# Performance work log

Hardware: AMD Instinct MI355X
Metric: run time of the kernel (lower is better)

Reference implementation:

```python
import jax, jax.numpy as jnp
import numpy as np

D_K = 16

def setup_inputs() -> dict:
    key = jax.random.key(0)
    kq, kk, kv, km, kb = jax.random.split(key, 5)
    B, H, S, d = 8, 16, 1024, D_K
    Q = jax.random.normal(kq, (B, H, S, d), dtype=jnp.float32)
    K = jax.random.normal(kk, (B, H, S, d), dtype=jnp.float32)
    V = jax.random.normal(kv, (B, H, S, d), dtype=jnp.float32)
    attn_mask = jax.random.randint(km, (B, 1, S, S), 0, 2).astype(jnp.bool_)
    MD_bias = jax.random.normal(kb, (B, 1, S, S), dtype=jnp.float32)
    return {"Q": Q, "K": K, "V": V, "attn_mask": attn_mask, "MD_bias": MD_bias}

def reference(Q, K, V, attn_mask, MD_bias):
    # scores: [B,H,S,S] = Q K^T / sqrt(d_k) + MD_bias, masked to -1e9
    scale = 1.0 / np.sqrt(D_K).astype(np.float32)
    scores = jnp.einsum('bhqd,bhkd->bhqk', Q, K) * scale + MD_bias
    scores = jnp.where(attn_mask, jnp.float32(-1e9), scores)
    attn = jax.nn.softmax(scores, axis=-1)
    context = jnp.einsum('bhqk,bhkd->bhqd', attn, V)
    return context
```

## Files before the change

### kernel.cpp

```cpp
#include <hip/hip_runtime.h>
#include <hip/hip_fp16.h>
#include <math.h>

#define SEQ    1024
#define DK     16
#define NHEAD  16
#define NBATCH 8
#define LOG2E  1.4426950408889634f

#define CH     128
#define NCH    (SEQ / CH)
#define KHL_STRIDE 72
#define VT_STRIDE  272
#define KHL_CH (CH * KHL_STRIDE)
#define VT_CH  (DK * VT_STRIDE)
#define BUF_SZ (KHL_CH + VT_CH)

typedef __attribute__((ext_vector_type(4))) short  short4v;
typedef __attribute__((ext_vector_type(4))) float  float4v;
typedef __attribute__((ext_vector_type(2))) unsigned int uint2v;

static __device__ __forceinline__ float fast_exp2(float x) {
#if __has_builtin(__builtin_amdgcn_exp2f)
    return __builtin_amdgcn_exp2f(x);
#else
    return exp2f(x);
#endif
}

static __device__ __forceinline__ float4v mfma16(short4v a, short4v b, float4v c) {
#if __has_builtin(__builtin_amdgcn_mfma_f32_16x16x16bf16_1k)
    return __builtin_amdgcn_mfma_f32_16x16x16bf16_1k(a, b, c, 0, 0, 0);
#else
    float4v d = c;
    asm volatile("v_mfma_f32_16x16x16_bf16 %0, %1, %2, %0" : "+v"(d) : "v"(a), "v"(b));
    return d;
#endif
}

static __device__ __forceinline__ unsigned bf16_rne(float x) {
    unsigned u = __float_as_uint(x);
    return (u + 0x7FFFu + ((u >> 16) & 1u)) >> 16;
}
static __device__ __forceinline__ float bf16_to_f(unsigned b) {
    return __uint_as_float(b << 16);
}
static __device__ __forceinline__ short4v bc_s4(unsigned lo, unsigned hi) {
    uint2v u; u.x = lo; u.y = hi;
    return __builtin_bit_cast(short4v, u);
}
static __device__ __forceinline__ unsigned h2pack(int m0, float b0, int m1, float b1) {
    const __half2 a = __floats2half2_rn(m0 ? -60000.f : b0 * LOG2E,
                                        m1 ? -60000.f : b1 * LOG2E);
    return __builtin_bit_cast(unsigned, a);
}

__global__ __launch_bounds__(256)
void prep_all(const float* __restrict__ K, const float* __restrict__ V,
              const int* __restrict__ mask, const float* __restrict__ bias,
              uint4* __restrict__ KHL, short* __restrict__ Vt,
              uint4* __restrict__ biasp) {
    const int blk = blockIdx.x;
    if (blk < 2048) {
        const int i4 = blk * 256 + threadIdx.x;
        const float4 k = ((const float4*)K)[i4];
        const float w[4] = {k.x, k.y, k.z, k.w};
        unsigned hh[4], ll[4];
        #pragma unroll
        for (int e = 0; e < 4; ++e) {
            hh[e] = bf16_rne(w[e]);
            ll[e] = bf16_rne(w[e] - bf16_to_f(hh[e]));
        }
        uint4 o;
        o.x = hh[0] | (hh[1] << 16);
        o.y = hh[2] | (hh[3] << 16);
        o.z = ll[0] | (ll[1] << 16);
        o.w = ll[2] | (ll[3] << 16);
        KHL[i4] = o;
    } else if (blk < 4096) {
        __shared__ float Vs[64][17];
        const int t  = threadIdx.x;
        const int bb = blk - 2048;
        const int bh = bb >> 4;
        const int s0 = (bb & 15) * 64;
        {
            const int row = t >> 2, c4 = t & 3;
            const float4 v = ((const float4*)V)[((size_t)bh * SEQ + s0 + row) * 4 + c4];
            Vs[row][c4 * 4 + 0] = v.x; Vs[row][c4 * 4 + 1] = v.y;
            Vs[row][c4 * 4 + 2] = v.z; Vs[row][c4 * 4 + 3] = v.w;
        }
        __syncthreads();
        const int d = t >> 4, sg = t & 15;
        short4v o;
        #pragma unroll
        for (int i = 0; i < 4; ++i) o[i] = (short)bf16_rne(Vs[sg * 4 + i][d]);
        ((short4v*)Vt)[(((size_t)bh * DK + d) * SEQ + s0) / 4 + sg] = o;
    } else {
        __shared__ uint4 BsT[64][16];
        const int t    = threadIdx.x;
        const int blk2 = blk - 4096;
        const int b    = blk2 >> 7;
        const int qt64 = (blk2 >> 3) & 15;
        const int c    = blk2 & 7;
        #pragma unroll
        for (int i = 0; i < 8; ++i) {
            const int idx = t + i * 256;
            const int row = idx >> 5;
            const int c4  = idx & 31;
            const size_t ga = ((size_t)b * SEQ + qt64 * 64 + row) * SEQ + c * 128 + c4 * 4;
            const float4 bv = *(const float4*)(bias + ga);
            const int4   mv = *(const int4*)(mask + ga);
            uint2 u;
            u.x = h2pack(mv.x, bv.x, mv.y, bv.y);
            u.y = h2pack(mv.z, bv.z, mv.w, bv.w);
            const int j = c4 >> 1;
            ((uint2*)&BsT[row][j ^ (row & 15)])[c4 & 1] = u;
        }
        __syncthreads();
        const int w = t >> 6, lane = t & 63, n = lane & 15, g = lane >> 4;
        #pragma unroll
        for (int tp = 0; tp < 4; ++tp) {
            const int j = tp * 4 + g;
            const uint4 v = BsT[w * 16 + n][j ^ n];
            const size_t ob = ((((size_t)(b * 16 + qt64) * 4 + w) * 8 + c) * 4 + tp) * 64 + lane;
            biasp[ob] = v;
        }
    }
}

__global__ __launch_bounds__(256, 4)
void sdpa_flash(const float* __restrict__ Q, const uint4* __restrict__ KHL,
                const short* __restrict__ Vt, const uint4* __restrict__ biasp,
                float* __restrict__ out) {
    __shared__ __align__(16) char smem[2][BUF_SZ];

    const int tid  = threadIdx.x;
    const int wave = tid >> 6;
    const int lane = tid & 63;
    const int n    = lane & 15;
    const int g    = lane >> 4;
    const int permn = ((n >> 2) << 3) | (n & 3);

    const int b  = blockIdx.x & 7;
    const int j  = blockIdx.x >> 3;
    const int qt = j & 7;
    const int h  = j >> 3;
    const int q0 = qt * 128;

    const size_t bh = (size_t)b * NHEAD + h;

    short4v qh[2], ql[2];
    size_t  bfbase[2];
    #pragma unroll
    for (int f = 0; f < 2; ++f) {
        const int qrow = q0 + f * 64 + wave * 16 + n;
        const float4 qv = *(const float4*)(Q + (bh * SEQ + qrow) * DK + g * 4);
        const float qsc = 0.25f * LOG2E;
        const float v[4] = {qv.x * qsc, qv.y * qsc, qv.z * qsc, qv.w * qsc};
        #pragma unroll
        for (int e = 0; e < 4; ++e) {
            const unsigned hu = bf16_rne(v[e]);
            qh[f][e] = (short)hu;
            ql[f][e] = (short)bf16_rne(v[e] - bf16_to_f(hu));
        }
        bfbase[f] = (((size_t)(b * 16 + qt * 2 + f) * 4 + wave) * 32) * 64 + lane;
    }

    const uint4* KHLh = KHL + bh * SEQ * 4;
    const uint4* VtH  = (const uint4*)(Vt + bh * DK * SEQ);

    float4v acc[2];
    float   lsum[2] = {0.f, 0.f};
    acc[0] = (float4v){0.f, 0.f, 0.f, 0.f};
    acc[1] = (float4v){0.f, 0.f, 0.f, 0.f};

    uint4 st0, st1, st2;
    {
        st0 = KHLh[tid];
        st1 = KHLh[256 + tid];
        st2 = VtH[(tid >> 4) * 128 + (tid & 15)];
        char* s = smem[0];
        *(uint4*)(s + (tid >> 2) * KHL_STRIDE + (tid & 3) * 16) = st0;
        const int e = tid + 256;
        *(uint4*)(s + (e >> 2) * KHL_STRIDE + (e & 3) * 16) = st1;
        *(uint4*)(s + KHL_CH + (tid >> 4) * VT_STRIDE + (tid & 15) * 16) = st2;
    }
    __syncthreads();

    for (int c = 0; c < NCH; ++c) {
        const int cur = c & 1;
        if (c < NCH - 1) {
            const uint4* kg = KHLh + (c + 1) * 512;
            st0 = kg[tid];
            st1 = kg[256 + tid];
            st2 = VtH[(tid >> 4) * 128 + (c + 1) * 16 + (tid & 15)];
        }
        uint4 bb[2][4];
        #pragma unroll
        for (int f = 0; f < 2; ++f)
            #pragma unroll
            for (int tp = 0; tp < 4; ++tp)
                bb[f][tp] = biasp[bfbase[f] + (size_t)(c * 4 + tp) * 64];

        const char* khl = smem[cur];
        const char* vtl = smem[cur] + KHL_CH;

        #pragma unroll
        for (int tp = 0; tp < 4; ++tp) {
            const int rowA = tp * 32 + permn;
            const uint4 kA = *(const uint4*)(khl + rowA * KHL_STRIDE + g * 16);
            const uint4 kB = *(const uint4*)(khl + (rowA + 4) * KHL_STRIDE + g * 16);
            const uint4 vv = *(const uint4*)(vtl + n * VT_STRIDE + tp * 64 + g * 16);
            const short4v khiA = bc_s4(kA.x, kA.y), kloA = bc_s4(kA.z, kA.w);
            const short4v khiB = bc_s4(kB.x, kB.y), kloB = bc_s4(kB.z, kB.w);
            const short4v vtA  = bc_s4(vv.x, vv.y), vtB  = bc_s4(vv.z, vv.w);

            #pragma unroll
            for (int f = 0; f < 2; ++f) {
                {
                    const float2 f01 = __half22float2(__builtin_bit_cast(__half2, bb[f][tp].x));
                    const float2 f23 = __half22float2(__builtin_bit_cast(__half2, bb[f][tp].y));
                    float4v s; s[0] = f01.x; s[1] = f01.y; s[2] = f23.x; s[3] = f23.y;
                    s = mfma16(khiA, qh[f], s);
                    s = mfma16(kloA, qh[f], s);
                    s = mfma16(khiA, ql[f], s);
                    const float p0 = fast_exp2(s[0]), p1 = fast_exp2(s[1]);
                    const float p2 = fast_exp2(s[2]), p3 = fast_exp2(s[3]);
                    lsum[f] += (p0 + p1) + (p2 + p3);
                    const unsigned u0 = __float_as_uint(p0) + 0x8000u;
                    const unsigned u1 = __float_as_uint(p1) + 0x8000u;
                    const unsigned u2 = __float_as_uint(p2) + 0x8000u;
                    const unsigned u3 = __float_as_uint(p3) + 0x8000u;
                    const short4v pf = bc_s4((u1 & 0xFFFF0000u) | (u0 >> 16),
                                             (u3 & 0xFFFF0000u) | (u2 >> 16));
                    acc[f] = mfma16(pf, vtA, acc[f]);
                }
                {
                    const float2 f01 = __half22float2(__builtin_bit_cast(__half2, bb[f][tp].z));
                    const float2 f23 = __half22float2(__builtin_bit_cast(__half2, bb[f][tp].w));
                    float4v s; s[0] = f01.x; s[1] = f01.y; s[2] = f23.x; s[3] = f23.y;
                    s = mfma16(khiB, qh[f], s);
                    s = mfma16(kloB, qh[f], s);
                    s = mfma16(khiB, ql[f], s);
                    const float p0 = fast_exp2(s[0]), p1 = fast_exp2(s[1]);
                    const float p2 = fast_exp2(s[2]), p3 = fast_exp2(s[3]);
                    lsum[f] += (p0 + p1) + (p2 + p3);
                    const unsigned u0 = __float_as_uint(p0) + 0x8000u;
                    const unsigned u1 = __float_as_uint(p1) + 0x8000u;
                    const unsigned u2 = __float_as_uint(p2) + 0x8000u;
                    const unsigned u3 = __float_as_uint(p3) + 0x8000u;
                    const short4v pf = bc_s4((u1 & 0xFFFF0000u) | (u0 >> 16),
                                             (u3 & 0xFFFF0000u) | (u2 >> 16));
                    acc[f] = mfma16(pf, vtB, acc[f]);
                }
            }
        }

        if (c < NCH - 1) {
            char* s = smem[cur ^ 1];
            *(uint4*)(s + (tid >> 2) * KHL_STRIDE + (tid & 3) * 16) = st0;
            const int e = tid + 256;
            *(uint4*)(s + (e >> 2) * KHL_STRIDE + (e & 3) * 16) = st1;
            *(uint4*)(s + KHL_CH + (tid >> 4) * VT_STRIDE + (tid & 15) * 16) = st2;
        }
        __syncthreads();
    }

    #pragma unroll
    for (int f = 0; f < 2; ++f) {
        float l = lsum[f];
        l += __shfl_xor(l, 16, 64);
        l += __shfl_xor(l, 32, 64);
        const float inv = 1.0f / l;
        const size_t obase = bh * SEQ + q0 + f * 64 + wave * 16;
        #pragma unroll
        for (int r = 0; r < 4; ++r) {
            const float invr = __shfl(inv, 4 * g + r, 64);
            out[(obase + 4 * g + r) * DK + n] = acc[f][r] * invr;
        }
    }
}

#define FTQ 256
#define FTK 32
__global__ __launch_bounds__(256, 2)
void sdpa_fallback(const float* __restrict__ Q, const float* __restrict__ K,
                   const float* __restrict__ V, const int* __restrict__ mask,
                   const float* __restrict__ bias, float* __restrict__ out) {
    __shared__ float Ks[FTK][DK];
    __shared__ float Vs[FTK][DK];
    __shared__ float Bsf[FTQ][FTK + 1];

    const int tid = threadIdx.x;
    const int blk = blockIdx.x;
    const int h   = blk & (NHEAD - 1);
    const int qt  = (blk >> 4) & 3;
    const int b   = blk >> 6;
    const int q0  = qt * FTQ;
    const float qscale = 0.25f * LOG2E;
    const size_t bh = (size_t)b * NHEAD + h;

    float Qr[DK];
    {
        const float4* q4 = (const float4*)(Q + (bh * SEQ + q0 + tid) * DK);
        #pragma unroll
        for (int i = 0; i < 4; ++i) {
            float4 v = q4[i];
            Qr[4*i+0] = v.x * qscale; Qr[4*i+1] = v.y * qscale;
            Qr[4*i+2] = v.z * qscale; Qr[4*i+3] = v.w * qscale;
        }
    }
    float acc[DK];
    #pragma unroll
    for (int d = 0; d < DK; ++d) acc[d] = 0.0f;
    float l = 0.0f;

    const float* Kbase = K + bh * SEQ * DK;
    const float* Vbase = V + bh * SEQ * DK;
    const float* Bbase = bias + ((size_t)b * SEQ + q0) * SEQ;
    const int*   Mbase = mask + ((size_t)b * SEQ + q0) * SEQ;

    for (int t = 0; t < SEQ / FTK; ++t) {
        const int k0 = t * FTK;
        if (tid < 128) {
            float4 kv = ((const float4*)(Kbase + (size_t)k0 * DK))[tid];
            float4 vv = ((const float4*)(Vbase + (size_t)k0 * DK))[tid];
            ((float4*)&Ks[0][0])[tid] = kv;
            ((float4*)&Vs[0][0])[tid] = vv;
        }
        #pragma unroll
        for (int i = 0; i < 8; ++i) {
            int e4 = tid + i * 256, row = e4 >> 3, c4 = e4 & 7;
            const float4 bv = *(const float4*)(Bbase + (size_t)row * SEQ + k0 + c4 * 4);
            const int4   mv = *(const int4*)  (Mbase + (size_t)row * SEQ + k0 + c4 * 4);
            float* dst = &Bsf[row][c4 * 4];
            dst[0] = mv.x ? -1e9f : bv.x * LOG2E;
            dst[1] = mv.y ? -1e9f : bv.y * LOG2E;
            dst[2] = mv.z ? -1e9f : bv.z * LOG2E;
            dst[3] = mv.w ? -1e9f : bv.w * LOG2E;
        }
        __syncthreads();
        #pragma unroll 4
        for (int kk = 0; kk < FTK; ++kk) {
            float s = Bsf[tid][kk];
            const float4 k0v = *(const float4*)&Ks[kk][0];
            const float4 k1v = *(const float4*)&Ks[kk][4];
            const float4 k2v = *(const float4*)&Ks[kk][8];
            const float4 k3v = *(const float4*)&Ks[kk][12];
            s = fmaf(Qr[0],  k0v.x, s); s = fmaf(Qr[1],  k0v.y, s);
            s = fmaf(Qr[2],  k0v.z, s); s = fmaf(Qr[3],  k0v.w, s);
            s = fmaf(Qr[4],  k1v.x, s); s = fmaf(Qr[5],  k1v.y, s);
            s = fmaf(Qr[6],  k1v.z, s); s = fmaf(Qr[7],  k1v.w, s);
            s = fmaf(Qr[8],  k2v.x, s); s = fmaf(Qr[9],  k2v.y, s);
            s = fmaf(Qr[10], k2v.z, s); s = fmaf(Qr[11], k2v.w, s);
            s = fmaf(Qr[12], k3v.x, s); s = fmaf(Qr[13], k3v.y, s);
            s = fmaf(Qr[14], k3v.z, s); s = fmaf(Qr[15], k3v.w, s);
            float p = fast_exp2(s);
            l += p;
            const float4 v0 = *(const float4*)&Vs[kk][0];
            const float4 v1 = *(const float4*)&Vs[kk][4];
            const float4 v2 = *(const float4*)&Vs[kk][8];
            const float4 v3 = *(const float4*)&Vs[kk][12];
            acc[0]  = fmaf(p, v0.x, acc[0]);  acc[1]  = fmaf(p, v0.y, acc[1]);
            acc[2]  = fmaf(p, v0.z, acc[2]);  acc[3]  = fmaf(p, v0.w, acc[3]);
            acc[4]  = fmaf(p, v1.x, acc[4]);  acc[5]  = fmaf(p, v1.y, acc[5]);
            acc[6]  = fmaf(p, v1.z, acc[6]);  acc[7]  = fmaf(p, v1.w, acc[7]);
            acc[8]  = fmaf(p, v2.x, acc[8]);  acc[9]  = fmaf(p, v2.y, acc[9]);
            acc[10] = fmaf(p, v2.z, acc[10]); acc[11] = fmaf(p, v2.w, acc[11]);
            acc[12] = fmaf(p, v3.x, acc[12]); acc[13] = fmaf(p, v3.y, acc[13]);
            acc[14] = fmaf(p, v3.z, acc[14]); acc[15] = fmaf(p, v3.w, acc[15]);
        }
        __syncthreads();
    }
    const float inv = 1.0f / l;
    float4* o4 = (float4*)(out + (bh * SEQ + q0 + tid) * DK);
    #pragma unroll
    for (int i = 0; i < 4; ++i) {
        float4 v;
        v.x = acc[4*i+0] * inv; v.y = acc[4*i+1] * inv;
        v.z = acc[4*i+2] * inv; v.w = acc[4*i+3] * inv;
        o4[i] = v;
    }
}

extern "C" void kernel_launch(void* const* d_in, const int* in_sizes, int n_in,
                              void* d_out, int out_size, void* d_ws, size_t ws_size,
                              hipStream_t stream) {
    const float* Q    = (const float*)d_in[0];
    const float* K    = (const float*)d_in[1];
    const float* V    = (const float*)d_in[2];
    const int*   mask = (const int*)  d_in[3];
    const float* bias = (const float*)d_in[4];
    float* out = (float*)d_out;

    const size_t nKeys    = (size_t)NBATCH * NHEAD * SEQ;
    const size_t khlBytes = nKeys * 64;
    const size_t vtBytes  = nKeys * DK * sizeof(short);
    const size_t bpBytes  = (size_t)NBATCH * SEQ * SEQ * 2;
    const size_t need     = khlBytes + vtBytes + bpBytes;

    if (ws_size >= need) {
        char* w = (char*)d_ws;
        uint4* KHL   = (uint4*)(w);
        short* Vt    = (short*)(w + khlBytes);
        uint4* biasp = (uint4*)(w + khlBytes + vtBytes);

        prep_all<<<5120, 256, 0, stream>>>(K, V, mask, bias, KHL, Vt, biasp);
        sdpa_flash<<<1024, 256, 0, stream>>>(Q, KHL, Vt, biasp, out);
    } else {
        sdpa_fallback<<<NBATCH * NHEAD * (SEQ / FTQ), FTQ, 0, stream>>>(Q, K, V, mask, bias, out);
    }
}
```

Measured before the change: 169.1 us.

## Fuse K/V bf16 conversion into flash kernel staging; shrink bias prep kernel

Removes the K hi/lo split and V transpose passes from the prep kernel. The flash kernel now loads fp32 K and V directly, converts them to bf16 (hi/lo for K, transposed for V) while staging each chunk into LDS, and no longer round-trips through workspace. The prep kernel now only packs mask and bias, with 2048 smaller blocks and a narrower swizzled LDS tile. The softmax probabilities now use the packed bf16 convert instruction where available. The cost is extra conversion ALU work inside the main loop, plus double the fp32 K/V global reads in the flash kernel, since each head's K/V is reloaded by 8 query-tile blocks.

Measured after the change: 164.3 us. 2.8% less time.

```diff
diff --git a/kernel.cpp b/kernel.cpp
--- a/kernel.cpp
+++ b/kernel.cpp
@@ -17,6 +17,7 @@
 #define BUF_SZ (KHL_CH + VT_CH)
 
 typedef __attribute__((ext_vector_type(4))) short  short4v;
+typedef __attribute__((ext_vector_type(2))) short  short2v;
 typedef __attribute__((ext_vector_type(4))) float  float4v;
 typedef __attribute__((ext_vector_type(2))) unsigned int uint2v;
 
@@ -45,6 +46,14 @@
 static __device__ __forceinline__ float bf16_to_f(unsigned b) {
     return __uint_as_float(b << 16);
 }
+static __device__ __forceinline__ unsigned pk_bf16(float a, float b) {
+#if __has_builtin(__builtin_amdgcn_cvt_pk_bf16_f32)
+    short2v r = __builtin_amdgcn_cvt_pk_bf16_f32(a, b);
+    return __builtin_bit_cast(unsigned, r);
+#else
+    return bf16_rne(a) | (bf16_rne(b) << 16);
+#endif
+}
 static __device__ __forceinline__ short4v bc_s4(unsigned lo, unsigned hi) {
     uint2v u; u.x = lo; u.y = hi;
     return __builtin_bit_cast(short4v, u);
@@ -56,81 +65,47 @@
 }
 
 __global__ __launch_bounds__(256)
-void prep_all(const float* __restrict__ K, const float* __restrict__ V,
-              const int* __restrict__ mask, const float* __restrict__ bias,
-              uint4* __restrict__ KHL, short* __restrict__ Vt,
-              uint4* __restrict__ biasp) {
-    const int blk = blockIdx.x;
-    if (blk < 2048) {
-        const int i4 = blk * 256 + threadIdx.x;
-        const float4 k = ((const float4*)K)[i4];
-        const float w[4] = {k.x, k.y, k.z, k.w};
-        unsigned hh[4], ll[4];
-        #pragma unroll
-        for (int e = 0; e < 4; ++e) {
-            hh[e] = bf16_rne(w[e]);
-            ll[e] = bf16_rne(w[e] - bf16_to_f(hh[e]));
-        }
-        uint4 o;
-        o.x = hh[0] | (hh[1] << 16);
-        o.y = hh[2] | (hh[3] << 16);
-        o.z = ll[0] | (ll[1] << 16);
-        o.w = ll[2] | (ll[3] << 16);
-        KHL[i4] = o;
-    } else if (blk < 4096) {
-        __shared__ float Vs[64][17];
-        const int t  = threadIdx.x;
-        const int bb = blk - 2048;
-        const int bh = bb >> 4;
-        const int s0 = (bb & 15) * 64;
-        {
-            const int row = t >> 2, c4 = t & 3;
-            const float4 v = ((const float4*)V)[((size_t)bh * SEQ + s0 + row) * 4 + c4];
-            Vs[row][c4 * 4 + 0] = v.x; Vs[row][c4 * 4 + 1] = v.y;
-            Vs[row][c4 * 4 + 2] = v.z; Vs[row][c4 * 4 + 3] = v.w;
-        }
-        __syncthreads();
-        const int d = t >> 4, sg = t & 15;
-        short4v o;
-        #pragma unroll
-        for (int i = 0; i < 4; ++i) o[i] = (short)bf16_rne(Vs[sg * 4 + i][d]);
-        ((short4v*)Vt)[(((size_t)bh * DK + d) * SEQ + s0) / 4 + sg] = o;
-    } else {
-        __shared__ uint4 BsT[64][16];
-        const int t    = threadIdx.x;
-        const int blk2 = blk - 4096;
-        const int b    = blk2 >> 7;
-        const int qt64 = (blk2 >> 3) & 15;
-        const int c    = blk2 & 7;
-        #pragma unroll
-        for (int i = 0; i < 8; ++i) {
-            const int idx = t + i * 256;
-            const int row = idx >> 5;
-            const int c4  = idx & 31;
-            const size_t ga = ((size_t)b * SEQ + qt64 * 64 + row) * SEQ + c * 128 + c4 * 4;
-            const float4 bv = *(const float4*)(bias + ga);
-            const int4   mv = *(const int4*)(mask + ga);
-            uint2 u;
-            u.x = h2pack(mv.x, bv.x, mv.y, bv.y);
-            u.y = h2pack(mv.z, bv.z, mv.w, bv.w);
-            const int j = c4 >> 1;
-            ((uint2*)&BsT[row][j ^ (row & 15)])[c4 & 1] = u;
-        }
-        __syncthreads();
-        const int w = t >> 6, lane = t & 63, n = lane & 15, g = lane >> 4;
-        #pragma unroll
-        for (int tp = 0; tp < 4; ++tp) {
-            const int j = tp * 4 + g;
-            const uint4 v = BsT[w * 16 + n][j ^ n];
-            const size_t ob = ((((size_t)(b * 16 + qt64) * 4 + w) * 8 + c) * 4 + tp) * 64 + lane;
-            biasp[ob] = v;
-        }
+void prep_bias(const int* __restrict__ mask, const float* __restrict__ bias,
+               uint4* __restrict__ biasp) {
+    __shared__ uint4 BsT[64][9];
+    const int t    = threadIdx.x;
+    const int blk  = blockIdx.x;
+    const int b    = blk >> 8;
+    const int qt64 = (blk >> 4) & 15;
+    const int c    = (blk >> 1) & 7;
+    const int half = blk & 1;
+    const int kb   = c * 128 + half * 64;
+
+    #pragma unroll
+    for (int i = 0; i < 4; ++i) {
+        const int idx = t + i * 256;
+        const int row = idx >> 4;
+        const int c4  = idx & 15;
+        const size_t ga = ((size_t)b * SEQ + qt64 * 64 + row) * SEQ + kb + c4 * 4;
+        const float4 bv = *(const float4*)(bias + ga);
+        const int4   mv = *(const int4*)(mask + ga);
+        uint2 u;
+        u.x = h2pack(mv.x, bv.x, mv.y, bv.y);
+        u.y = h2pack(mv.z, bv.z, mv.w, bv.w);
+        const int j = c4 >> 1;
+        ((uint2*)&BsT[row][j ^ (row & 7)])[c4 & 1] = u;
+    }
+    __syncthreads();
+    const int w = t >> 6, lane = t & 63, n = lane & 15, g = lane >> 4;
+    const int row = w * 16 + n;
+    #pragma unroll
+    for (int tpl = 0; tpl < 2; ++tpl) {
+        const int tp = half * 2 + tpl;
+        const int jj = tpl * 4 + g;
+        const uint4 v = BsT[row][jj ^ (row & 7)];
+        const size_t ob = ((((size_t)(b * 16 + qt64) * 4 + w) * 8 + c) * 4 + tp) * 64 + lane;
+        biasp[ob] = v;
     }
 }
 
 __global__ __launch_bounds__(256, 4)
-void sdpa_flash(const float* __restrict__ Q, const uint4* __restrict__ KHL,
-                const short* __restrict__ Vt, const uint4* __restrict__ biasp,
+void sdpa_flash(const float* __restrict__ Q, const float* __restrict__ K,
+                const float* __restrict__ V, const uint4* __restrict__ biasp,
                 float* __restrict__ out) {
     __shared__ __align__(16) char smem[2][BUF_SZ];
 
@@ -166,34 +141,67 @@
         bfbase[f] = (((size_t)(b * 16 + qt * 2 + f) * 4 + wave) * 32) * 64 + lane;
     }
 
-    const uint4* KHLh = KHL + bh * SEQ * 4;
-    const uint4* VtH  = (const uint4*)(Vt + bh * DK * SEQ);
+    const float4* Kf4 = (const float4*)(K + bh * SEQ * DK);
+    const float4* Vf4 = (const float4*)(V + bh * SEQ * DK);
+
+    const int sp = tid >> 2;
+    const int cc = tid & 3;
 
     float4v acc[2];
     float   lsum[2] = {0.f, 0.f};
     acc[0] = (float4v){0.f, 0.f, 0.f, 0.f};
     acc[1] = (float4v){0.f, 0.f, 0.f, 0.f};
 
-    uint4 st0, st1, st2;
-    {
-        st0 = KHLh[tid];
-        st1 = KHLh[256 + tid];
-        st2 = VtH[(tid >> 4) * 128 + (tid & 15)];
-        char* s = smem[0];
-        *(uint4*)(s + (tid >> 2) * KHL_STRIDE + (tid & 3) * 16) = st0;
-        const int e = tid + 256;
-        *(uint4*)(s + (e >> 2) * KHL_STRIDE + (e & 3) * 16) = st1;
-        *(uint4*)(s + KHL_CH + (tid >> 4) * VT_STRIDE + (tid & 15) * 16) = st2;
-    }
+    float4 kst0, kst1, vst0, vst1;
+    kst0 = Kf4[tid];
+    kst1 = Kf4[256 + tid];
+    vst0 = Vf4[(2 * sp) * 4 + cc];
+    vst1 = Vf4[(2 * sp + 1) * 4 + cc];
+
+    auto stage = [&](char* s) {
+        {
+            const float w0[4] = {kst0.x, kst0.y, kst0.z, kst0.w};
+            uint4 o;
+            o.x = pk_bf16(w0[0], w0[1]);
+            o.y = pk_bf16(w0[2], w0[3]);
+            o.z = pk_bf16(w0[0] - bf16_to_f(o.x & 0xFFFFu),
+                          w0[1] - bf16_to_f(o.x >> 16));
+            o.w = pk_bf16(w0[2] - bf16_to_f(o.y & 0xFFFFu),
+                          w0[3] - bf16_to_f(o.y >> 16));
+            *(uint4*)(s + (tid >> 2) * KHL_STRIDE + (tid & 3) * 16) = o;
+            const float w1[4] = {kst1.x, kst1.y, kst1.z, kst1.w};
+            uint4 p;
+            p.x = pk_bf16(w1[0], w1[1]);
+            p.y = pk_bf16(w1[2], w1[3]);
+            p.z = pk_bf16(w1[0] - bf16_to_f(p.x & 0xFFFFu),
+                          w1[1] - bf16_to_f(p.x >> 16));
+            p.w = pk_bf16(w1[2] - bf16_to_f(p.y & 0xFFFFu),
+                          w1[3] - bf16_to_f(p.y >> 16));
+            const int e = tid + 256;
+            *(uint4*)(s + (e >> 2) * KHL_STRIDE + (e & 3) * 16) = p;
+        }
+        {
+            const float a0[4] = {vst0.x, vst0.y, vst0.z, vst0.w};
+            const float a1[4] = {vst1.x, vst1.y, vst1.z, vst1.w};
+            #pragma unroll
+            for (int dp = 0; dp < 4; ++dp) {
+                const unsigned pr = pk_bf16(a0[dp], a1[dp]);
+                *(unsigned*)(s + KHL_CH + (cc * 4 + dp) * VT_STRIDE + sp * 4) = pr;
+            }
+        }
+    };
+
+    stage(smem[0]);
     __syncthreads();
 
     for (int c = 0; c < NCH; ++c) {
         const int cur = c & 1;
         if (c < NCH - 1) {
-            const uint4* kg = KHLh + (c + 1) * 512;
-            st0 = kg[tid];
-            st1 = kg[256 + tid];
-            st2 = VtH[(tid >> 4) * 128 + (c + 1) * 16 + (tid & 15)];
+            const int o4 = (c + 1) * 512;
+            kst0 = Kf4[o4 + tid];
+            kst1 = Kf4[o4 + 256 + tid];
+            vst0 = Vf4[o4 + (2 * sp) * 4 + cc];
+            vst1 = Vf4[o4 + (2 * sp + 1) * 4 + cc];
         }
         uint4 bb[2][4];
         #pragma unroll
@@ -227,12 +235,7 @@
                     const float p0 = fast_exp2(s[0]), p1 = fast_exp2(s[1]);
                     const float p2 = fast_exp2(s[2]), p3 = fast_exp2(s[3]);
                     lsum[f] += (p0 + p1) + (p2 + p3);
-                    const unsigned u0 = __float_as_uint(p0) + 0x8000u;
-                    const unsigned u1 = __float_as_uint(p1) + 0x8000u;
-                    const unsigned u2 = __float_as_uint(p2) + 0x8000u;
-                    const unsigned u3 = __float_as_uint(p3) + 0x8000u;
-                    const short4v pf = bc_s4((u1 & 0xFFFF0000u) | (u0 >> 16),
-                                             (u3 & 0xFFFF0000u) | (u2 >> 16));
+                    const short4v pf = bc_s4(pk_bf16(p0, p1), pk_bf16(p2, p3));
                     acc[f] = mfma16(pf, vtA, acc[f]);
                 }
                 {
@@ -245,24 +248,13 @@
                     const float p0 = fast_exp2(s[0]), p1 = fast_exp2(s[1]);
                     const float p2 = fast_exp2(s[2]), p3 = fast_exp2(s[3]);
                     lsum[f] += (p0 + p1) + (p2 + p3);
-                    const unsigned u0 = __float_as_uint(p0) + 0x8000u;
-                    const unsigned u1 = __float_as_uint(p1) + 0x8000u;
-                    const unsigned u2 = __float_as_uint(p2) + 0x8000u;
-                    const unsigned u3 = __float_as_uint(p3) + 0x8000u;
-                    const short4v pf = bc_s4((u1 & 0xFFFF0000u) | (u0 >> 16),
-                                             (u3 & 0xFFFF0000u) | (u2 >> 16));
+                    const short4v pf = bc_s4(pk_bf16(p0, p1), pk_bf16(p2, p3));
                     acc[f] = mfma16(pf, vtB, acc[f]);
                 }
             }
         }
 
-        if (c < NCH - 1) {
-            char* s = smem[cur ^ 1];
-            *(uint4*)(s + (tid >> 2) * KHL_STRIDE + (tid & 3) * 16) = st0;
-            const int e = tid + 256;
-            *(uint4*)(s + (e >> 2) * KHL_STRIDE + (e & 3) * 16) = st1;
-            *(uint4*)(s + KHL_CH + (tid >> 4) * VT_STRIDE + (tid & 15) * 16) = st2;
-        }
+        if (c < NCH - 1) stage(smem[cur ^ 1]);
         __syncthreads();
     }
 
@@ -393,20 +385,12 @@
     const float* bias = (const float*)d_in[4];
     float* out = (float*)d_out;
 
-    const size_t nKeys    = (size_t)NBATCH * NHEAD * SEQ;
-    const size_t khlBytes = nKeys * 64;
-    const size_t vtBytes  = nKeys * DK * sizeof(short);
-    const size_t bpBytes  = (size_t)NBATCH * SEQ * SEQ * 2;
-    const size_t need     = khlBytes + vtBytes + bpBytes;
-
-    if (ws_size >= need) {
-        char* w = (char*)d_ws;
-        uint4* KHL   = (uint4*)(w);
-        short* Vt    = (short*)(w + khlBytes);
-        uint4* biasp = (uint4*)(w + khlBytes + vtBytes);
-
-        prep_all<<<5120, 256, 0, stream>>>(K, V, mask, bias, KHL, Vt, biasp);
-        sdpa_flash<<<1024, 256, 0, stream>>>(Q, KHL, Vt, biasp, out);
+    const size_t bpBytes = (size_t)NBATCH * SEQ * SEQ * 2;
+
+    if (ws_size >= bpBytes) {
+        uint4* biasp = (uint4*)d_ws;
+        prep_bias<<<2048, 256, 0, stream>>>(mask, bias, biasp);
+        sdpa_flash<<<1024, 256, 0, stream>>>(Q, K, V, biasp, out);
     } else {
         sdpa_fallback<<<NBATCH * NHEAD * (SEQ / FTQ), FTQ, 0, stream>>>(Q, K, V, mask, bias, out);
     }
```

## Halve flash tile sizes, compute row sums via MFMA, use packed bf16 convert

Applied to the files above, without the earlier changes.

The flash kernel now handles 64 query rows per block instead of 128 and streams 64-key chunks instead of 128. This doubles the grid and raises the occupancy target to 8 blocks per CU, while reducing registers and shared memory per block. The softmax denominator is now accumulated by an extra MFMA against a ones vector rather than by VALU adds plus cross-lane shuffles. Probabilities are packed with a hardware cvt_pk_bf16 instruction where available. The bias-prep blocks are split in half to match the new layout, which adds more prep blocks and more per-chunk barriers.

After: 200.3 us. 1.18x slower.

```diff
diff --git a/kernel.cpp b/kernel.cpp
--- a/kernel.cpp
+++ b/kernel.cpp
@@ -8,15 +8,16 @@
 #define NBATCH 8
 #define LOG2E  1.4426950408889634f
 
-#define CH     128
+#define CH     64
 #define NCH    (SEQ / CH)
 #define KHL_STRIDE 72
-#define VT_STRIDE  272
+#define VT_STRIDE  144
 #define KHL_CH (CH * KHL_STRIDE)
 #define VT_CH  (DK * VT_STRIDE)
 #define BUF_SZ (KHL_CH + VT_CH)
 
 typedef __attribute__((ext_vector_type(4))) short  short4v;
+typedef __attribute__((ext_vector_type(2))) short  short2v;
 typedef __attribute__((ext_vector_type(4))) float  float4v;
 typedef __attribute__((ext_vector_type(2))) unsigned int uint2v;
 
@@ -44,6 +45,14 @@
 }
 static __device__ __forceinline__ float bf16_to_f(unsigned b) {
     return __uint_as_float(b << 16);
+}
+static __device__ __forceinline__ unsigned pk_bf16(float a, float b) {
+#if __has_builtin(__builtin_amdgcn_cvt_pk_bf16_f32)
+    short2v r = __builtin_amdgcn_cvt_pk_bf16_f32(a, b);
+    return __builtin_bit_cast(unsigned, r);
+#else
+    return bf16_rne(a) | (bf16_rne(b) << 16);
+#endif
 }
 static __device__ __forceinline__ short4v bc_s4(unsigned lo, unsigned hi) {
     uint2v u; u.x = lo; u.y = hi;
@@ -65,17 +74,11 @@
         const int i4 = blk * 256 + threadIdx.x;
         const float4 k = ((const float4*)K)[i4];
         const float w[4] = {k.x, k.y, k.z, k.w};
-        unsigned hh[4], ll[4];
-        #pragma unroll
-        for (int e = 0; e < 4; ++e) {
-            hh[e] = bf16_rne(w[e]);
-            ll[e] = bf16_rne(w[e] - bf16_to_f(hh[e]));
-        }
         uint4 o;
-        o.x = hh[0] | (hh[1] << 16);
-        o.y = hh[2] | (hh[3] << 16);
-        o.z = ll[0] | (ll[1] << 16);
-        o.w = ll[2] | (ll[3] << 16);
+        o.x = pk_bf16(w[0], w[1]);
+        o.y = pk_bf16(w[2], w[3]);
+        o.z = pk_bf16(w[0] - bf16_to_f(o.x & 0xFFFFu), w[1] - bf16_to_f(o.x >> 16));
+        o.w = pk_bf16(w[2] - bf16_to_f(o.y & 0xFFFFu), w[3] - bf16_to_f(o.y >> 16));
         KHL[i4] = o;
     } else if (blk < 4096) {
         __shared__ float Vs[64][17];
@@ -96,39 +99,44 @@
         for (int i = 0; i < 4; ++i) o[i] = (short)bf16_rne(Vs[sg * 4 + i][d]);
         ((short4v*)Vt)[(((size_t)bh * DK + d) * SEQ + s0) / 4 + sg] = o;
     } else {
-        __shared__ uint4 BsT[64][16];
+        __shared__ uint4 BsT[64][9];
         const int t    = threadIdx.x;
         const int blk2 = blk - 4096;
-        const int b    = blk2 >> 7;
-        const int qt64 = (blk2 >> 3) & 15;
-        const int c    = blk2 & 7;
-        #pragma unroll
-        for (int i = 0; i < 8; ++i) {
+        const int b    = blk2 >> 8;
+        const int qt64 = (blk2 >> 4) & 15;
+        const int c    = (blk2 >> 1) & 7;
+        const int half = blk2 & 1;
+        const int kb   = c * 128 + half * 64;
+
+        #pragma unroll
+        for (int i = 0; i < 4; ++i) {
             const int idx = t + i * 256;
-            const int row = idx >> 5;
-            const int c4  = idx & 31;
-            const size_t ga = ((size_t)b * SEQ + qt64 * 64 + row) * SEQ + c * 128 + c4 * 4;
+            const int row = idx >> 4;
+            const int c4  = idx & 15;
+            const size_t ga = ((size_t)b * SEQ + qt64 * 64 + row) * SEQ + kb + c4 * 4;
             const float4 bv = *(const float4*)(bias + ga);
             const int4   mv = *(const int4*)(mask + ga);
             uint2 u;
             u.x = h2pack(mv.x, bv.x, mv.y, bv.y);
             u.y = h2pack(mv.z, bv.z, mv.w, bv.w);
             const int j = c4 >> 1;
-            ((uint2*)&BsT[row][j ^ (row & 15)])[c4 & 1] = u;
+            ((uint2*)&BsT[row][j ^ (row & 7)])[c4 & 1] = u;
         }
         __syncthreads();
         const int w = t >> 6, lane = t & 63, n = lane & 15, g = lane >> 4;
-        #pragma unroll
-        for (int tp = 0; tp < 4; ++tp) {
-            const int j = tp * 4 + g;
-            const uint4 v = BsT[w * 16 + n][j ^ n];
+        const int row = w * 16 + n;
+        #pragma unroll
+        for (int tpl = 0; tpl < 2; ++tpl) {
+            const int tp = half * 2 + tpl;
+            const int jj = tpl * 4 + g;
+            const uint4 v = BsT[row][jj ^ (row & 7)];
             const size_t ob = ((((size_t)(b * 16 + qt64) * 4 + w) * 8 + c) * 4 + tp) * 64 + lane;
             biasp[ob] = v;
         }
     }
 }
 
-__global__ __launch_bounds__(256, 4)
+__global__ __launch_bounds__(256, 8)
 void sdpa_flash(const float* __restrict__ Q, const uint4* __restrict__ KHL,
                 const short* __restrict__ Vt, const uint4* __restrict__ biasp,
                 float* __restrict__ out) {
@@ -143,70 +151,64 @@
 
     const int b  = blockIdx.x & 7;
     const int j  = blockIdx.x >> 3;
-    const int qt = j & 7;
-    const int h  = j >> 3;
-    const int q0 = qt * 128;
-
-    const size_t bh = (size_t)b * NHEAD + h;
-
-    short4v qh[2], ql[2];
-    size_t  bfbase[2];
-    #pragma unroll
-    for (int f = 0; f < 2; ++f) {
-        const int qrow = q0 + f * 64 + wave * 16 + n;
+    const int qt = j & 15;
+    const int h  = j >> 4;
+    const int q0 = qt * 64;
+
+    const size_t bh   = (size_t)b * NHEAD + h;
+    const int    qrow = q0 + wave * 16 + n;
+
+    short4v qh, ql;
+    {
         const float4 qv = *(const float4*)(Q + (bh * SEQ + qrow) * DK + g * 4);
         const float qsc = 0.25f * LOG2E;
         const float v[4] = {qv.x * qsc, qv.y * qsc, qv.z * qsc, qv.w * qsc};
         #pragma unroll
         for (int e = 0; e < 4; ++e) {
             const unsigned hu = bf16_rne(v[e]);
-            qh[f][e] = (short)hu;
-            ql[f][e] = (short)bf16_rne(v[e] - bf16_to_f(hu));
-        }
-        bfbase[f] = (((size_t)(b * 16 + qt * 2 + f) * 4 + wave) * 32) * 64 + lane;
-    }
+            qh[e] = (short)hu;
+            ql[e] = (short)bf16_rne(v[e] - bf16_to_f(hu));
+        }
+    }
+    const size_t bfbase = (((size_t)(b * 16 + qt) * 4 + wave) * 32) * 64 + lane;
 
     const uint4* KHLh = KHL + bh * SEQ * 4;
     const uint4* VtH  = (const uint4*)(Vt + bh * DK * SEQ);
 
-    float4v acc[2];
-    float   lsum[2] = {0.f, 0.f};
-    acc[0] = (float4v){0.f, 0.f, 0.f, 0.f};
-    acc[1] = (float4v){0.f, 0.f, 0.f, 0.f};
-
-    uint4 st0, st1, st2;
-    {
-        st0 = KHLh[tid];
-        st1 = KHLh[256 + tid];
-        st2 = VtH[(tid >> 4) * 128 + (tid & 15)];
-        char* s = smem[0];
-        *(uint4*)(s + (tid >> 2) * KHL_STRIDE + (tid & 3) * 16) = st0;
-        const int e = tid + 256;
-        *(uint4*)(s + (e >> 2) * KHL_STRIDE + (e & 3) * 16) = st1;
-        *(uint4*)(s + KHL_CH + (tid >> 4) * VT_STRIDE + (tid & 15) * 16) = st2;
-    }
+    const int vd = tid >> 3, vc = tid & 7;
+
+    float4v acc   = (float4v){0.f, 0.f, 0.f, 0.f};
+    float4v acc_l = (float4v){0.f, 0.f, 0.f, 0.f};
+    const short4v kOnes = {(short)0x3F80, (short)0x3F80, (short)0x3F80, (short)0x3F80};
+
+    uint4 kst, vst;
+    kst = KHLh[tid];
+    if (tid < 128) vst = VtH[vd * 128 + vc];
+
+    auto stage = [&](char* s) {
+        *(uint4*)(s + (tid >> 2) * KHL_STRIDE + (tid & 3) * 16) = kst;
+        if (tid < 128)
+            *(uint4*)(s + KHL_CH + vd * VT_STRIDE + vc * 16) = vst;
+    };
+
+    stage(smem[0]);
     __syncthreads();
 
     for (int c = 0; c < NCH; ++c) {
         const int cur = c & 1;
         if (c < NCH - 1) {
-            const uint4* kg = KHLh + (c + 1) * 512;
-            st0 = kg[tid];
-            st1 = kg[256 + tid];
-            st2 = VtH[(tid >> 4) * 128 + (c + 1) * 16 + (tid & 15)];
-        }
-        uint4 bb[2][4];
-        #pragma unroll
-        for (int f = 0; f < 2; ++f)
-            #pragma unroll
-            for (int tp = 0; tp < 4; ++tp)
-                bb[f][tp] = biasp[bfbase[f] + (size_t)(c * 4 + tp) * 64];
+            kst = KHLh[(c + 1) * 256 + tid];
+            if (tid < 128) vst = VtH[vd * 128 + (c + 1) * 8 + vc];
+        }
+        uint4 bb[2];
+        bb[0] = biasp[bfbase + (size_t)(c * 2 + 0) * 64];
+        bb[1] = biasp[bfbase + (size_t)(c * 2 + 1) * 64];
 
         const char* khl = smem[cur];
         const char* vtl = smem[cur] + KHL_CH;
 
         #pragma unroll
-        for (int tp = 0; tp < 4; ++tp) {
+        for (int tp = 0; tp < 2; ++tp) {
             const int rowA = tp * 32 + permn;
             const uint4 kA = *(const uint4*)(khl + rowA * KHL_STRIDE + g * 16);
             const uint4 kB = *(const uint4*)(khl + (rowA + 4) * KHL_STRIDE + g * 16);
@@ -215,69 +217,43 @@
             const short4v khiB = bc_s4(kB.x, kB.y), kloB = bc_s4(kB.z, kB.w);
             const short4v vtA  = bc_s4(vv.x, vv.y), vtB  = bc_s4(vv.z, vv.w);
 
-            #pragma unroll
-            for (int f = 0; f < 2; ++f) {
-                {
-                    const float2 f01 = __half22float2(__builtin_bit_cast(__half2, bb[f][tp].x));
-                    const float2 f23 = __half22float2(__builtin_bit_cast(__half2, bb[f][tp].y));
-                    float4v s; s[0] = f01.x; s[1] = f01.y; s[2] = f23.x; s[3] = f23.y;
-                    s = mfma16(khiA, qh[f], s);
-                    s = mfma16(kloA, qh[f], s);
-                    s = mfma16(khiA, ql[f], s);
-                    const float p0 = fast_exp2(s[0]), p1 = fast_exp2(s[1]);
-                    const float p2 = fast_exp2(s[2]), p3 = fast_exp2(s[3]);
-                    lsum[f] += (p0 + p1) + (p2 + p3);
-                    const unsigned u0 = __float_as_uint(p0) + 0x8000u;
-                    const unsigned u1 = __float_as_uint(p1) + 0x8000u;
-                    const unsigned u2 = __float_as_uint(p2) + 0x8000u;
-                    const unsigned u3 = __float_as_uint(p3) + 0x8000u;
-                    const short4v pf = bc_s4((u1 & 0xFFFF0000u) | (u0 >> 16),
-                                             (u3 & 0xFFFF0000u) | (u2 >> 16));
-                    acc[f] = mfma16(pf, vtA, acc[f]);
-                }
-                {
-                    const float2 f01 = __half22float2(__builtin_bit_cast(__half2, bb[f][tp].z));
-                    const float2 f23 = __half22float2(__builtin_bit_cast(__half2, bb[f][tp].w));
-                    float4v s; s[0] = f01.x; s[1] = f01.y; s[2] = f23.x; s[3] = f23.y;
-                    s = mfma16(khiB, qh[f], s);
-                    s = mfma16(kloB, qh[f], s);
-                    s = mfma16(khiB, ql[f], s);
-                    const float p0 = fast_exp2(s[0]), p1 = fast_exp2(s[1]);
-                    const float p2 = fast_exp2(s[2]), p3 = fast_exp2(s[3]);
-                    lsum[f] += (p0 + p1) + (p2 + p3);
-                    const unsigned u0 = __float_as_uint(p0) + 0x8000u;
-                    const unsigned u1 = __float_as_uint(p1) + 0x8000u;
-                    const unsigned u2 = __float_as_uint(p2) + 0x8000u;
-                    const unsigned u3 = __float_as_uint(p3) + 0x8000u;
-                    const short4v pf = bc_s4((u1 & 0xFFFF0000u) | (u0 >> 16),
-                                             (u3 & 0xFFFF0000u) | (u2 >> 16));
-                    acc[f] = mfma16(pf, vtB, acc[f]);
-                }
+            {
+                const float2 f01 = __half22float2(__builtin_bit_cast(__half2, bb[tp].x));
+                const float2 f23 = __half22float2(__builtin_bit_cast(__half2, bb[tp].y));
+                float4v s; s[0] = f01.x; s[1] = f01.y; s[2] = f23.x; s[3] = f23.y;
+                s = mfma16(khiA, qh, s);
+                s = mfma16(kloA, qh, s);
+                s = mfma16(khiA, ql, s);
+                const float p0 = fast_exp2(s[0]), p1 = fast_exp2(s[1]);
+                const float p2 = fast_exp2(s[2]), p3 = fast_exp2(s[3]);
+                const short4v pf = bc_s4(pk_bf16(p0, p1), pk_bf16(p2, p3));
+                acc   = mfma16(pf, vtA,   acc);
+                acc_l = mfma16(pf, kOnes, acc_l);
             }
-        }
-
-        if (c < NCH - 1) {
-            char* s = smem[cur ^ 1];
-            *(uint4*)(s + (tid >> 2) * KHL_STRIDE + (tid & 3) * 16) = st0;
-            const int e = tid + 256;
-            *(uint4*)(s + (e >> 2) * KHL_STRIDE + (e & 3) * 16) = st1;
-            *(uint4*)(s + KHL_CH + (tid >> 4) * VT_STRIDE + (tid & 15) * 16) = st2;
-        }
-        __syncthreads();
-    }
-
+            {
+                const float2 f01 = __half22float2(__builtin_bit_cast(__half2, bb[tp].z));
+                const float2 f23 = __half22float2(__builtin_bit_cast(__half2, bb[tp].w));
+                float4v s; s[0] = f01.x; s[1] = f01.y; s[2] = f23.x; s[3] = f23.y;
+                s = mfma16(khiB, qh, s);
+                s = mfma16(kloB, qh, s);
+                s = mfma16(khiB, ql, s);
+                const float p0 = fast_exp2(s[0]), p1 = fast_exp2(s[1]);
+                const float p2 = fast_exp2(s[2]), p3 = fast_exp2(s[3]);
+                const short4v pf = bc_s4(pk_bf16(p0, p1), pk_bf16(p2, p3));
+                acc   = mfma16(pf, vtB,   acc);
+                acc_l = mfma16(pf, kOnes, acc_l);
+            }
+        }
+
+        if (c < NCH - 1) stage(smem[cur ^ 1]);
+        __syncthreads();
+    }
+
+    const size_t obase = bh * SEQ + q0 + wave * 16;
     #pragma unroll
-    for (int f = 0; f < 2; ++f) {
-        float l = lsum[f];
-        l += __shfl_xor(l, 16, 64);
-        l += __shfl_xor(l, 32, 64);
-        const float inv = 1.0f / l;
-        const size_t obase = bh * SEQ + q0 + f * 64 + wave * 16;
-        #pragma unroll
-        for (int r = 0; r < 4; ++r) {
-            const float invr = __shfl(inv, 4 * g + r, 64);
-            out[(obase + 4 * g + r) * DK + n] = acc[f][r] * invr;
-        }
+    for (int r = 0; r < 4; ++r) {
+        const float inv = 1.0f / acc_l[r];
+        out[(obase + 4 * g + r) * DK + n] = acc[r] * inv;
     }
 }
 
@@ -405,8 +381,8 @@
         short* Vt    = (short*)(w + khlBytes);
         uint4* biasp = (uint4*)(w + khlBytes + vtBytes);
 
-        prep_all<<<5120, 256, 0, stream>>>(K, V, mask, bias, KHL, Vt, biasp);
-        sdpa_flash<<<1024, 256, 0, stream>>>(Q, KHL, Vt, biasp, out);
+        prep_all<<<6144, 256, 0, stream>>>(K, V, mask, bias, KHL, Vt, biasp);
+        sdpa_flash<<<2048, 256, 0, stream>>>(Q, KHL, Vt, biasp, out);
     } else {
         sdpa_fallback<<<NBATCH * NHEAD * (SEQ / FTQ), FTQ, 0, stream>>>(Q, K, V, mask, bias, out);
     }
```

## Use 16x16x32 bf16 MFMA for PV, compute row sums via MFMA, rebalance prep kernel

Applied to the files above, without the earlier changes.

The P·V product now uses one 16x16x32 bf16 MFMA per tile pair instead of two 16x16x16 ones. The softmax denominator is accumulated by a second MFMA against a ones vector, which removes the scalar adds and cross-lane shuffles. Probabilities are packed with the hardware bf16 convert instruction. The prep kernel is restructured: bias/mask blocks come first and are split into halves, and each K/V block handles more work, cutting the grid from 5120 to 3072 blocks. The ones-vector MFMA adds matrix work and accumulator registers, and the denominator now sums bf16-rounded probabilities rather than fp32 ones.

Result: no change. 167.2 us (-1.1%).

```diff
diff --git a/kernel.cpp b/kernel.cpp
--- a/kernel.cpp
+++ b/kernel.cpp
@@ -17,6 +17,8 @@
 #define BUF_SZ (KHL_CH + VT_CH)
 
 typedef __attribute__((ext_vector_type(4))) short  short4v;
+typedef __attribute__((ext_vector_type(8))) short  short8v;
+typedef __attribute__((ext_vector_type(2))) short  short2v;
 typedef __attribute__((ext_vector_type(4))) float  float4v;
 typedef __attribute__((ext_vector_type(2))) unsigned int uint2v;
 
@@ -38,12 +40,31 @@
 #endif
 }
 
+static __device__ __forceinline__ float4v mfma32(short8v a, short8v b, float4v c) {
+#if __has_builtin(__builtin_amdgcn_mfma_f32_16x16x32_bf16)
+    return __builtin_amdgcn_mfma_f32_16x16x32_bf16(a, b, c, 0, 0, 0);
+#else
+    short4v a0 = {a[0], a[1], a[2], a[3]}, a1 = {a[4], a[5], a[6], a[7]};
+    short4v b0 = {b[0], b[1], b[2], b[3]}, b1 = {b[4], b[5], b[6], b[7]};
+    c = mfma16(a0, b0, c);
+    return mfma16(a1, b1, c);
+#endif
+}
+
 static __device__ __forceinline__ unsigned bf16_rne(float x) {
     unsigned u = __float_as_uint(x);
     return (u + 0x7FFFu + ((u >> 16) & 1u)) >> 16;
 }
 static __device__ __forceinline__ float bf16_to_f(unsigned b) {
     return __uint_as_float(b << 16);
+}
+static __device__ __forceinline__ unsigned pk_bf16(float a, float b) {
+#if __has_builtin(__builtin_amdgcn_cvt_pk_bf16_f32)
+    short2v r = __builtin_amdgcn_cvt_pk_bf16_f32(a, b);
+    return __builtin_bit_cast(unsigned, r);
+#else
+    return bf16_rne(a) | (bf16_rne(b) << 16);
+#endif
 }
 static __device__ __forceinline__ short4v bc_s4(unsigned lo, unsigned hi) {
     uint2v u; u.x = lo; u.y = hi;
@@ -61,69 +82,74 @@
               uint4* __restrict__ KHL, short* __restrict__ Vt,
               uint4* __restrict__ biasp) {
     const int blk = blockIdx.x;
+    const int t   = threadIdx.x;
     if (blk < 2048) {
-        const int i4 = blk * 256 + threadIdx.x;
-        const float4 k = ((const float4*)K)[i4];
-        const float w[4] = {k.x, k.y, k.z, k.w};
-        unsigned hh[4], ll[4];
-        #pragma unroll
-        for (int e = 0; e < 4; ++e) {
-            hh[e] = bf16_rne(w[e]);
-            ll[e] = bf16_rne(w[e] - bf16_to_f(hh[e]));
-        }
-        uint4 o;
-        o.x = hh[0] | (hh[1] << 16);
-        o.y = hh[2] | (hh[3] << 16);
-        o.z = ll[0] | (ll[1] << 16);
-        o.w = ll[2] | (ll[3] << 16);
-        KHL[i4] = o;
-    } else if (blk < 4096) {
-        __shared__ float Vs[64][17];
-        const int t  = threadIdx.x;
-        const int bb = blk - 2048;
-        const int bh = bb >> 4;
-        const int s0 = (bb & 15) * 64;
-        {
-            const int row = t >> 2, c4 = t & 3;
-            const float4 v = ((const float4*)V)[((size_t)bh * SEQ + s0 + row) * 4 + c4];
-            Vs[row][c4 * 4 + 0] = v.x; Vs[row][c4 * 4 + 1] = v.y;
-            Vs[row][c4 * 4 + 2] = v.z; Vs[row][c4 * 4 + 3] = v.w;
-        }
-        __syncthreads();
-        const int d = t >> 4, sg = t & 15;
-        short4v o;
-        #pragma unroll
-        for (int i = 0; i < 4; ++i) o[i] = (short)bf16_rne(Vs[sg * 4 + i][d]);
-        ((short4v*)Vt)[(((size_t)bh * DK + d) * SEQ + s0) / 4 + sg] = o;
-    } else {
-        __shared__ uint4 BsT[64][16];
-        const int t    = threadIdx.x;
-        const int blk2 = blk - 4096;
-        const int b    = blk2 >> 7;
-        const int qt64 = (blk2 >> 3) & 15;
-        const int c    = blk2 & 7;
-        #pragma unroll
-        for (int i = 0; i < 8; ++i) {
+        __shared__ uint4 BsT[64][9];
+        const int b    = blk >> 8;
+        const int qt64 = (blk >> 4) & 15;
+        const int c    = (blk >> 1) & 7;
+        const int half = blk & 1;
+        const int kb   = c * 128 + half * 64;
+        #pragma unroll
+        for (int i = 0; i < 4; ++i) {
             const int idx = t + i * 256;
-            const int row = idx >> 5;
-            const int c4  = idx & 31;
-            const size_t ga = ((size_t)b * SEQ + qt64 * 64 + row) * SEQ + c * 128 + c4 * 4;
+            const int row = idx >> 4;
+            const int c4  = idx & 15;
+            const size_t ga = ((size_t)b * SEQ + qt64 * 64 + row) * SEQ + kb + c4 * 4;
             const float4 bv = *(const float4*)(bias + ga);
             const int4   mv = *(const int4*)(mask + ga);
             uint2 u;
             u.x = h2pack(mv.x, bv.x, mv.y, bv.y);
             u.y = h2pack(mv.z, bv.z, mv.w, bv.w);
-            const int j = c4 >> 1;
-            ((uint2*)&BsT[row][j ^ (row & 15)])[c4 & 1] = u;
+            const int jj = c4 >> 1;
+            ((uint2*)&BsT[row][jj ^ (row & 7)])[c4 & 1] = u;
         }
         __syncthreads();
         const int w = t >> 6, lane = t & 63, n = lane & 15, g = lane >> 4;
-        #pragma unroll
-        for (int tp = 0; tp < 4; ++tp) {
-            const int j = tp * 4 + g;
-            const uint4 v = BsT[w * 16 + n][j ^ n];
+        const int row = w * 16 + n;
+        #pragma unroll
+        for (int tpl = 0; tpl < 2; ++tpl) {
+            const int tp = half * 2 + tpl;
+            const int jj = tpl * 4 + g;
+            const uint4 v = BsT[row][jj ^ (row & 7)];
             const size_t ob = ((((size_t)(b * 16 + qt64) * 4 + w) * 8 + c) * 4 + tp) * 64 + lane;
             biasp[ob] = v;
+        }
+    } else if (blk < 2560) {
+        const int base = (blk - 2048) * 1024;
+        #pragma unroll
+        for (int i = 0; i < 4; ++i) {
+            const int i4 = base + t + i * 256;
+            const float4 k = ((const float4*)K)[i4];
+            const float w[4] = {k.x, k.y, k.z, k.w};
+            uint4 o;
+            o.x = pk_bf16(w[0], w[1]);
+            o.y = pk_bf16(w[2], w[3]);
+            o.z = pk_bf16(w[0] - bf16_to_f(o.x & 0xFFFFu), w[1] - bf16_to_f(o.x >> 16));
+            o.w = pk_bf16(w[2] - bf16_to_f(o.y & 0xFFFFu), w[3] - bf16_to_f(o.y >> 16));
+            KHL[i4] = o;
+        }
+    } else {
+        __shared__ float Vs[64][17];
+        const int vb = blk - 2560;
+        const int bh = vb >> 2;
+        const int qq = vb & 3;
+        #pragma unroll
+        for (int st = 0; st < 4; ++st) {
+            const int s0 = qq * 256 + st * 64;
+            {
+                const int row = t >> 2, c4 = t & 3;
+                const float4 v = ((const float4*)V)[((size_t)bh * SEQ + s0 + row) * 4 + c4];
+                Vs[row][c4 * 4 + 0] = v.x; Vs[row][c4 * 4 + 1] = v.y;
+                Vs[row][c4 * 4 + 2] = v.z; Vs[row][c4 * 4 + 3] = v.w;
+            }
+            __syncthreads();
+            const int d = t >> 4, sg = t & 15;
+            short4v o;
+            #pragma unroll
+            for (int i = 0; i < 4; ++i) o[i] = (short)bf16_rne(Vs[sg * 4 + i][d]);
+            ((short4v*)Vt)[(((size_t)bh * DK + d) * SEQ + s0) / 4 + sg] = o;
+            __syncthreads();
         }
     }
 }
@@ -169,10 +195,13 @@
     const uint4* KHLh = KHL + bh * SEQ * 4;
     const uint4* VtH  = (const uint4*)(Vt + bh * DK * SEQ);
 
-    float4v acc[2];
-    float   lsum[2] = {0.f, 0.f};
-    acc[0] = (float4v){0.f, 0.f, 0.f, 0.f};
-    acc[1] = (float4v){0.f, 0.f, 0.f, 0.f};
+    float4v acc[2], accl[2];
+    acc[0]  = (float4v){0.f, 0.f, 0.f, 0.f};
+    acc[1]  = (float4v){0.f, 0.f, 0.f, 0.f};
+    accl[0] = (float4v){0.f, 0.f, 0.f, 0.f};
+    accl[1] = (float4v){0.f, 0.f, 0.f, 0.f};
+    const short8v ones8 = {(short)0x3F80, (short)0x3F80, (short)0x3F80, (short)0x3F80,
+                           (short)0x3F80, (short)0x3F80, (short)0x3F80, (short)0x3F80};
 
     uint4 st0, st1, st2;
     {
@@ -213,46 +242,37 @@
             const uint4 vv = *(const uint4*)(vtl + n * VT_STRIDE + tp * 64 + g * 16);
             const short4v khiA = bc_s4(kA.x, kA.y), kloA = bc_s4(kA.z, kA.w);
             const short4v khiB = bc_s4(kB.x, kB.y), kloB = bc_s4(kB.z, kB.w);
-            const short4v vtA  = bc_s4(vv.x, vv.y), vtB  = bc_s4(vv.z, vv.w);
+            const short8v vt8  = __builtin_bit_cast(short8v, vv);
 
             #pragma unroll
             for (int f = 0; f < 2; ++f) {
-                {
-                    const float2 f01 = __half22float2(__builtin_bit_cast(__half2, bb[f][tp].x));
-                    const float2 f23 = __half22float2(__builtin_bit_cast(__half2, bb[f][tp].y));
-                    float4v s; s[0] = f01.x; s[1] = f01.y; s[2] = f23.x; s[3] = f23.y;
-                    s = mfma16(khiA, qh[f], s);
-                    s = mfma16(kloA, qh[f], s);
-                    s = mfma16(khiA, ql[f], s);
-                    const float p0 = fast_exp2(s[0]), p1 = fast_exp2(s[1]);
-                    const float p2 = fast_exp2(s[2]), p3 = fast_exp2(s[3]);
-                    lsum[f] += (p0 + p1) + (p2 + p3);
-                    const unsigned u0 = __float_as_uint(p0) + 0x8000u;
-                    const unsigned u1 = __float_as_uint(p1) + 0x8000u;
-                    const unsigned u2 = __float_as_uint(p2) + 0x8000u;
-                    const unsigned u3 = __float_as_uint(p3) + 0x8000u;
-                    const short4v pf = bc_s4((u1 & 0xFFFF0000u) | (u0 >> 16),
-                                             (u3 & 0xFFFF0000u) | (u2 >> 16));
-                    acc[f] = mfma16(pf, vtA, acc[f]);
-                }
-                {
-                    const float2 f01 = __half22float2(__builtin_bit_cast(__half2, bb[f][tp].z));
-                    const float2 f23 = __half22float2(__builtin_bit_cast(__half2, bb[f][tp].w));
-                    float4v s; s[0] = f01.x; s[1] = f01.y; s[2] = f23.x; s[3] = f23.y;
-                    s = mfma16(khiB, qh[f], s);
-                    s = mfma16(kloB, qh[f], s);
-                    s = mfma16(khiB, ql[f], s);
-                    const float p0 = fast_exp2(s[0]), p1 = fast_exp2(s[1]);
-                    const float p2 = fast_exp2(s[2]), p3 = fast_exp2(s[3]);
-                    lsum[f] += (p0 + p1) + (p2 + p3);
-                    const unsigned u0 = __float_as_uint(p0) + 0x8000u;
-                    const unsigned u1 = __float_as_uint(p1) + 0x8000u;
-                    const unsigned u2 = __float_as_uint(p2) + 0x8000u;
-                    const unsigned u3 = __float_as_uint(p3) + 0x8000u;
-                    const short4v pf = bc_s4((u1 & 0xFFFF0000u) | (u0 >> 16),
-                                             (u3 & 0xFFFF0000u) | (u2 >> 16));
-                    acc[f] = mfma16(pf, vtB, acc[f]);
-                }
+                const float2 a01 = __half22float2(__builtin_bit_cast(__half2, bb[f][tp].x));
+                const float2 a23 = __half22float2(__builtin_bit_cast(__half2, bb[f][tp].y));
+                float4v sA; sA[0] = a01.x; sA[1] = a01.y; sA[2] = a23.x; sA[3] = a23.y;
+                sA = mfma16(khiA, qh[f], sA);
+                sA = mfma16(kloA, qh[f], sA);
+                sA = mfma16(khiA, ql[f], sA);
+                const float2 b01 = __half22float2(__builtin_bit_cast(__half2, bb[f][tp].z));
+                const float2 b23 = __half22float2(__builtin_bit_cast(__half2, bb[f][tp].w));
+                float4v sB; sB[0] = b01.x; sB[1] = b01.y; sB[2] = b23.x; sB[3] = b23.y;
+                sB = mfma16(khiB, qh[f], sB);
+                sB = mfma16(kloB, qh[f], sB);
+                sB = mfma16(khiB, ql[f], sB);
+
+                const float pA0 = fast_exp2(sA[0]), pA1 = fast_exp2(sA[1]);
+                const float pA2 = fast_exp2(sA[2]), pA3 = fast_exp2(sA[3]);
+                const float pB0 = fast_exp2(sB[0]), pB1 = fast_exp2(sB[1]);
+                const float pB2 = fast_exp2(sB[2]), pB3 = fast_exp2(sB[3]);
+
+                uint4 pu;
+                pu.x = pk_bf16(pA0, pA1);
+                pu.y = pk_bf16(pA2, pA3);
+                pu.z = pk_bf16(pB0, pB1);
+                pu.w = pk_bf16(pB2, pB3);
+                const short8v pf8 = __builtin_bit_cast(short8v, pu);
+
+                acc[f]  = mfma32(pf8, vt8,  acc[f]);
+                accl[f] = mfma32(pf8, ones8, accl[f]);
             }
         }
 
@@ -268,15 +288,10 @@
 
     #pragma unroll
     for (int f = 0; f < 2; ++f) {
-        float l = lsum[f];
-        l += __shfl_xor(l, 16, 64);
-        l += __shfl_xor(l, 32, 64);
-        const float inv = 1.0f / l;
         const size_t obase = bh * SEQ + q0 + f * 64 + wave * 16;
         #pragma unroll
         for (int r = 0; r < 4; ++r) {
-            const float invr = __shfl(inv, 4 * g + r, 64);
-            out[(obase + 4 * g + r) * DK + n] = acc[f][r] * invr;
+            out[(obase + 4 * g + r) * DK + n] = acc[f][r] / accl[f][r];
         }
     }
 }
@@ -405,7 +420,7 @@
         short* Vt    = (short*)(w + khlBytes);
         uint4* biasp = (uint4*)(w + khlBytes + vtBytes);
 
-        prep_all<<<5120, 256, 0, stream>>>(K, V, mask, bias, KHL, Vt, biasp);
+        prep_all<<<3072, 256, 0, stream>>>(K, V, mask, bias, KHL, Vt, biasp);
         sdpa_flash<<<1024, 256, 0, stream>>>(Q, KHL, Vt, biasp, out);
     } else {
         sdpa_fallback<<<NBATCH * NHEAD * (SEQ / FTQ), FTQ, 0, stream>>>(Q, K, V, mask, bias, out);
```
